# Kernel optimization log

Measured on AMD Instinct MI355X. Metric: run time of the kernel, lower is better.

The kernel has to match this reference:

```python
import jax, jax.numpy as jnp
import numpy as np

B, H, W, C = 4, 64, 64, 64
DK = C // 8  # key/query channels from Conv2D(filters=channels//8)


def setup_inputs() -> dict:
    key = jax.random.key(0)
    ks = jax.random.split(key, 4)
    x = jax.random.normal(ks[0], (B, H, W, C), dtype=jnp.float32)
    # he_normal-ish scale for 1x1 conv kernels (fan_in = C)
    s = np.sqrt(2.0 / C).astype(np.float32)
    Wf = jax.random.normal(ks[1], (C, DK), dtype=jnp.float32) * s
    Wg = jax.random.normal(ks[2], (C, DK), dtype=jnp.float32) * s
    Wh = jax.random.normal(ks[3], (C, C), dtype=jnp.float32) * s
    bf = jnp.zeros((DK,), dtype=jnp.float32)
    bg = jnp.zeros((DK,), dtype=jnp.float32)
    bh = jnp.zeros((C,), dtype=jnp.float32)
    return {"x": x, "Wf": Wf, "bf": bf, "Wg": Wg, "bg": bg, "Wh": Wh, "bh": bh}


def reference(x, Wf, bf, Wg, bg, Wh, bh):
    b, h, w, c = x.shape
    n = h * w
    xf = x.reshape(b, n, c)  # 1x1 conv == per-position linear over flattened spatial dims
    f = xf @ Wf + bf         # [B, N, DK]
    g = xf @ Wg + bg         # [B, N, DK]
    v = xf @ Wh + bh         # [B, N, C]
    # attention = softmax(g @ f^T) over keys (tf.nn.softmax default: last axis)
    scores = jnp.einsum('bnd,bmd->bnm', g, f)   # [B, N, N]
    attn = jax.nn.softmax(scores, axis=-1)
    out = jnp.einsum('bnm,bmc->bnc', attn, v)   # [B, N, C]
    return out
```

## Files before the change

### kernel.cpp

```cpp
#include <hip/hip_runtime.h>
#include <hip/hip_bf16.h>
#include <hip/hip_fp16.h>

typedef _Float16 half8_t  __attribute__((ext_vector_type(8)));
typedef short    short8_t __attribute__((ext_vector_type(8)));
typedef short    short4_t __attribute__((ext_vector_type(4)));
typedef float    f32x4    __attribute__((ext_vector_type(4)));

#define LOG2E 1.44269504088896f

__device__ __forceinline__ unsigned pack_bf16_2(float lo, float hi) {
  float2 f2; f2.x = lo; f2.y = hi;
  __hip_bfloat162 h2 = __float22bfloat162_rn(f2);
  return *reinterpret_cast<unsigned*>(&h2);
}

__global__ __launch_bounds__(512) void prep_kernel(
    const float* __restrict__ x,
    const float* __restrict__ Wf, const float* __restrict__ bf,
    const float* __restrict__ Wg, const float* __restrict__ bg,
    const float* __restrict__ Wh, const float* __restrict__ bh,
    _Float16* __restrict__ fh, _Float16* __restrict__ gh,
    unsigned short* __restrict__ vT)
{
  __shared__ _Float16 WtT[80 * 72];
  __shared__ float ball[80];
  const int t = threadIdx.x;

  {
    int c = t >> 3, d = t & 7;
    WtT[d * 72 + c]       = (_Float16)Wf[t];
    WtT[(8 + d) * 72 + c] = (_Float16)(Wg[t] * LOG2E);
  }
#pragma unroll
  for (int rep = 0; rep < 2; rep++) {
    int i4 = t + rep * 512;
    float4 wv4 = *(const float4*)(Wh + i4 * 4);
    int c  = i4 >> 4;
    int ch = (i4 & 15) * 4;
    WtT[(16 + ch + 0) * 72 + c] = (_Float16)wv4.x;
    WtT[(16 + ch + 1) * 72 + c] = (_Float16)wv4.y;
    WtT[(16 + ch + 2) * 72 + c] = (_Float16)wv4.z;
    WtT[(16 + ch + 3) * 72 + c] = (_Float16)wv4.w;
  }
  if (t < 80) ball[t] = (t < 8) ? bf[t] : (t < 16) ? bg[t - 8] * LOG2E : bh[t - 16];
  __syncthreads();

  const int lane = t & 63, wv = t >> 6;
  const int quad = lane >> 4, l15 = lane & 15;
  const int wr   = wv & 3;
  const int hsel = wv >> 2;
  const int p0  = blockIdx.x * 64;
  const int row = p0 + wr * 16 + l15;

  const float* xr = x + (size_t)row * 64 + quad * 8;
  float4 xa = *(const float4*)(xr);
  float4 xb = *(const float4*)(xr + 4);
  float4 xc = *(const float4*)(xr + 32);
  float4 xd = *(const float4*)(xr + 36);
  half8_t a0, a1;
  a0[0]=(_Float16)xa.x; a0[1]=(_Float16)xa.y; a0[2]=(_Float16)xa.z; a0[3]=(_Float16)xa.w;
  a0[4]=(_Float16)xb.x; a0[5]=(_Float16)xb.y; a0[6]=(_Float16)xb.z; a0[7]=(_Float16)xb.w;
  a1[0]=(_Float16)xc.x; a1[1]=(_Float16)xc.y; a1[2]=(_Float16)xc.z; a1[3]=(_Float16)xc.w;
  a1[4]=(_Float16)xd.x; a1[5]=(_Float16)xd.y; a1[6]=(_Float16)xd.z; a1[7]=(_Float16)xd.w;

  const f32x4 zc = {0.f, 0.f, 0.f, 0.f};
  const int b     = p0 >> 12;
  const int nbase = (p0 & 4095) + wr * 16 + quad * 4;
  const int kblock = nbase >> 5;
  const int r0     = nbase & 31;
  const int q8 = r0 >> 3, j8 = r0 & 7;
  const int slot0 = (j8 < 4) ? (q8 * 4 + j8) : (16 + q8 * 4 + (j8 - 4));
  const size_t fbase_out = ((size_t)b * 4096 + (kblock << 5) + slot0) * 8;
  const size_t gbase_out = ((size_t)p0 + wr * 16 + quad * 4) * 8;
  const size_t vbase_out = (((size_t)b * 128 + kblock) << 11) + r0;

  if (hsel == 0) {
    {
      const _Float16* wt = &WtT[l15 * 72 + quad * 8];
      half8_t b0 = *(const half8_t*)(wt);
      half8_t b1 = *(const half8_t*)(wt + 32);
      f32x4 d = __builtin_amdgcn_mfma_f32_16x16x32_f16(a0, b0, zc, 0, 0, 0);
      d = __builtin_amdgcn_mfma_f32_16x16x32_f16(a1, b1, d, 0, 0, 0);
      const float bias = ball[l15];
      if (l15 < 8) {
#pragma unroll
        for (int reg = 0; reg < 4; reg++)
          fh[fbase_out + (size_t)reg * 8 + l15] = (_Float16)(d[reg] + bias);
      } else {
#pragma unroll
        for (int reg = 0; reg < 4; reg++)
          gh[gbase_out + (size_t)reg * 8 + (l15 - 8)] = (_Float16)(d[reg] + bias);
      }
    }
#pragma unroll
    for (int nt = 1; nt < 3; nt++) {
      const int ch0 = nt * 16 + l15;
      const _Float16* wt = &WtT[ch0 * 72 + quad * 8];
      half8_t b0 = *(const half8_t*)(wt);
      half8_t b1 = *(const half8_t*)(wt + 32);
      f32x4 d = __builtin_amdgcn_mfma_f32_16x16x32_f16(a0, b0, zc, 0, 0, 0);
      d = __builtin_amdgcn_mfma_f32_16x16x32_f16(a1, b1, d, 0, 0, 0);
      const float bias = ball[ch0];
      const int vch = ch0 - 16;
      union { unsigned u[2]; short4_t s; } pk;
      pk.u[0] = pack_bf16_2(d[0] + bias, d[1] + bias);
      pk.u[1] = pack_bf16_2(d[2] + bias, d[3] + bias);
      *(short4_t*)(vT + vbase_out + (size_t)vch * 32) = pk.s;
    }
  } else {
#pragma unroll
    for (int nt = 3; nt < 5; nt++) {
      const int ch0 = nt * 16 + l15;
      const _Float16* wt = &WtT[ch0 * 72 + quad * 8];
      half8_t b0 = *(const half8_t*)(wt);
      half8_t b1 = *(const half8_t*)(wt + 32);
      f32x4 d = __builtin_amdgcn_mfma_f32_16x16x32_f16(a0, b0, zc, 0, 0, 0);
      d = __builtin_amdgcn_mfma_f32_16x16x32_f16(a1, b1, d, 0, 0, 0);
      const float bias = ball[ch0];
      const int vch = ch0 - 16;
      union { unsigned u[2]; short4_t s; } pk;
      pk.u[0] = pack_bf16_2(d[0] + bias, d[1] + bias);
      pk.u[1] = pack_bf16_2(d[2] + bias, d[3] + bias);
      *(short4_t*)(vT + vbase_out + (size_t)vch * 32) = pk.s;
    }
  }
}

__device__ __forceinline__ void compute_chunk(
    const half8_t& f0, const half8_t& f1,
    const short8_t& v0, const short8_t& v1,
    const short8_t& v2, const short8_t& v3,
    const half8_t (&gfrag)[4], const short8_t& ones8,
    f32x4 (&acc)[4][4], f32x4 (&acc4)[4])
{
  const f32x4 zc = {0.f, 0.f, 0.f, 0.f};
#pragma unroll
  for (int tt = 0; tt < 4; tt++) {
    f32x4 s0 = __builtin_amdgcn_mfma_f32_16x16x32_f16(f0, gfrag[tt], zc, 0, 0, 0);
    f32x4 s1 = __builtin_amdgcn_mfma_f32_16x16x32_f16(f1, gfrag[tt], zc, 0, 0, 0);
    float p00 = __builtin_amdgcn_exp2f(s0[0]), p01 = __builtin_amdgcn_exp2f(s0[1]);
    float p02 = __builtin_amdgcn_exp2f(s0[2]), p03 = __builtin_amdgcn_exp2f(s0[3]);
    float p10 = __builtin_amdgcn_exp2f(s1[0]), p11 = __builtin_amdgcn_exp2f(s1[1]);
    float p12 = __builtin_amdgcn_exp2f(s1[2]), p13 = __builtin_amdgcn_exp2f(s1[3]);
    union { unsigned u[4]; short8_t v; } pu;
    pu.u[0] = pack_bf16_2(p00, p01);
    pu.u[1] = pack_bf16_2(p02, p03);
    pu.u[2] = pack_bf16_2(p10, p11);
    pu.u[3] = pack_bf16_2(p12, p13);
    short8_t pfrag = pu.v;
    acc[tt][0] = __builtin_amdgcn_mfma_f32_16x16x32_bf16(v0, pfrag, acc[tt][0], 0, 0, 0);
    acc[tt][1] = __builtin_amdgcn_mfma_f32_16x16x32_bf16(v1, pfrag, acc[tt][1], 0, 0, 0);
    acc[tt][2] = __builtin_amdgcn_mfma_f32_16x16x32_bf16(v2, pfrag, acc[tt][2], 0, 0, 0);
    acc[tt][3] = __builtin_amdgcn_mfma_f32_16x16x32_bf16(v3, pfrag, acc[tt][3], 0, 0, 0);
    acc4[tt]   = __builtin_amdgcn_mfma_f32_16x16x32_bf16(ones8, pfrag, acc4[tt], 0, 0, 0);
  }
}

__global__ __launch_bounds__(512, 2) void attn_kernel(
    const _Float16* __restrict__ fh,
    const _Float16* __restrict__ gh,
    const unsigned short* __restrict__ vT,
    float* __restrict__ out)
{
  const int N    = 4096;
  const int lane = threadIdx.x & 63;
  const int w    = threadIdx.x >> 6;
  const int quad = lane >> 4;
  const int l15  = lane & 15;

  __shared__ float red[7][64][17];

  const int xcd = blockIdx.x & 7;
  const int b   = xcd >> 1;
  const int qg  = ((blockIdx.x >> 3) << 1) + (xcd & 1);
  const int q0  = qg * 64;
  const int kbase = w * 512;
  const int phase = (qg >> 1) & 15;

  const _Float16* fbase = fh + (size_t)b * N * 8;
  const _Float16* gbase = gh + (size_t)b * N * 8;
  const short*    vbat  = (const short*)vT + (size_t)b * 262144 + (l15 << 5) + (quad << 3);

  half8_t gfrag[4] = {{}, {}, {}, {}};
  if (quad == 0) {
#pragma unroll
    for (int tt = 0; tt < 4; tt++)
      gfrag[tt] = *(const half8_t*)(gbase + (size_t)(q0 + tt * 16 + l15) * 8);
  }

  const f32x4 zc = {0.f, 0.f, 0.f, 0.f};
  f32x4 acc[4][4];
  f32x4 acc4[4];
#pragma unroll
  for (int tt = 0; tt < 4; tt++) {
    acc4[tt] = zc;
#pragma unroll
    for (int ct = 0; ct < 4; ct++) acc[tt][ct] = zc;
  }

  short8_t ones8;
#pragma unroll
  for (int i = 0; i < 8; i++) ones8[i] = (short)0x3F80;

#define KOFF(j) (kbase + ((((j) + phase) & 15) << 5))
#define LOADC(k, F0, F1, V0, V1, V2, V3)                                  \
  {                                                                       \
    const int kk = (k);                                                   \
    if (quad == 0) {                                                      \
      F0 = *(const half8_t*)(fbase + (size_t)(kk + l15) * 8);             \
      F1 = *(const half8_t*)(fbase + (size_t)(kk + 16 + l15) * 8);        \
    }                                                                     \
    const short* vk = vbat + ((size_t)(kk >> 5) << 11);                   \
    V0 = *(const short8_t*)(vk);                                          \
    V1 = *(const short8_t*)(vk + 512);                                    \
    V2 = *(const short8_t*)(vk + 1024);                                   \
    V3 = *(const short8_t*)(vk + 1536);                                   \
  }

  half8_t  fA0 = {}, fA1 = {}, fB0 = {}, fB1 = {};
  half8_t  fC0 = {}, fC1 = {}, fD0 = {}, fD1 = {};
  short8_t vA0, vA1, vA2, vA3, vB0, vB1, vB2, vB3;
  short8_t vC0, vC1, vC2, vC3, vD0, vD1, vD2, vD3;

  LOADC(KOFF(0), fA0, fA1, vA0, vA1, vA2, vA3);
  LOADC(KOFF(1), fB0, fB1, vB0, vB1, vB2, vB3);

#pragma unroll 1
  for (int cc = 0; cc < 16; cc += 4) {
    LOADC(KOFF(cc + 2), fC0, fC1, vC0, vC1, vC2, vC3);
    LOADC(KOFF(cc + 3), fD0, fD1, vD0, vD1, vD2, vD3);
    compute_chunk(fA0, fA1, vA0, vA1, vA2, vA3, gfrag, ones8, acc, acc4);
    compute_chunk(fB0, fB1, vB0, vB1, vB2, vB3, gfrag, ones8, acc, acc4);
    if (cc + 4 < 16) {
      LOADC(KOFF(cc + 4), fA0, fA1, vA0, vA1, vA2, vA3);
      LOADC(KOFF(cc + 5), fB0, fB1, vB0, vB1, vB2, vB3);
    }
    compute_chunk(fC0, fC1, vC0, vC1, vC2, vC3, gfrag, ones8, acc, acc4);
    compute_chunk(fD0, fD1, vD0, vD1, vD2, vD3, gfrag, ones8, acc, acc4);
  }
#undef LOADC
#undef KOFF

#pragma unroll
  for (int tt = 0; tt < 4; tt++) {
    if (w > 0) {
      float* p = &red[w - 1][lane][0];
#pragma unroll
      for (int ct = 0; ct < 4; ct++)
#pragma unroll
        for (int reg = 0; reg < 4; reg++) p[ct * 4 + reg] = acc[tt][ct][reg];
      p[16] = acc4[tt][0];
    }
    __syncthreads();
    if (w == 0) {
#pragma unroll
      for (int ww = 0; ww < 7; ww++) {
        const float* p = &red[ww][lane][0];
#pragma unroll
        for (int reg = 0; reg < 4; reg++) {
          acc[tt][0][reg] += p[0 + reg];
          acc[tt][1][reg] += p[4 + reg];
          acc[tt][2][reg] += p[8 + reg];
          acc[tt][3][reg] += p[12 + reg];
        }
        acc4[tt][0] += p[16];
      }
    }
    if (tt < 3) __syncthreads();
  }

  if (w == 0) {
#pragma unroll
    for (int tt = 0; tt < 4; tt++) {
      const float inv = 1.0f / acc4[tt][0];
      float* ob = out + ((size_t)b * N + q0 + tt * 16 + l15) * 64 + (quad << 2);
      *(f32x4*)(ob)      = acc[tt][0] * inv;
      *(f32x4*)(ob + 16) = acc[tt][1] * inv;
      *(f32x4*)(ob + 32) = acc[tt][2] * inv;
      *(f32x4*)(ob + 48) = acc[tt][3] * inv;
    }
  }
}

extern "C" void kernel_launch(void* const* d_in, const int* in_sizes, int n_in,
                              void* d_out, int out_size, void* d_ws, size_t ws_size,
                              hipStream_t stream) {
  const float* x  = (const float*)d_in[0];
  const float* Wf = (const float*)d_in[1];
  const float* bf = (const float*)d_in[2];
  const float* Wg = (const float*)d_in[3];
  const float* bg = (const float*)d_in[4];
  const float* Wh = (const float*)d_in[5];
  const float* bh = (const float*)d_in[6];
  float* out = (float*)d_out;

  char* ws = (char*)d_ws;
  _Float16* fh = (_Float16*)ws;
  _Float16* gh = (_Float16*)(ws + 262144);
  unsigned short* vT = (unsigned short*)(ws + 524288);

  prep_kernel<<<256, 512, 0, stream>>>(x, Wf, bf, Wg, bg, Wh, bh, fh, gh, vT);
  attn_kernel<<<256, 512, 0, stream>>>(fh, gh, vT, out);
  attn_kernel<<<256, 512, 0, stream>>>(fh, gh, vT, out);
}
```

Baseline: 108.5 us.

## Fuse projection and attention into one kernel with a global atomic barrier

Merges the 1x1-conv projection kernel into the attention kernel, separated by a device-wide spin barrier on an atomic counter. The counter is reset with a memset each launch. This also drops the duplicated second attention launch. Shared memory is reused: a raw buffer first holds the transposed weights, then the reduction scratch. The barrier assumes all 256 blocks are co-resident, and a deadlock is possible if they are not.

```diff
diff --git a/kernel.cpp b/kernel.cpp
--- a/kernel.cpp
+++ b/kernel.cpp
@@ -13,118 +13,6 @@
   float2 f2; f2.x = lo; f2.y = hi;
   __hip_bfloat162 h2 = __float22bfloat162_rn(f2);
   return *reinterpret_cast<unsigned*>(&h2);
-}
-
-__global__ __launch_bounds__(512) void prep_kernel(
-    const float* __restrict__ x,
-    const float* __restrict__ Wf, const float* __restrict__ bf,
-    const float* __restrict__ Wg, const float* __restrict__ bg,
-    const float* __restrict__ Wh, const float* __restrict__ bh,
-    _Float16* __restrict__ fh, _Float16* __restrict__ gh,
-    unsigned short* __restrict__ vT)
-{
-  __shared__ _Float16 WtT[80 * 72];
-  __shared__ float ball[80];
-  const int t = threadIdx.x;
-
-  {
-    int c = t >> 3, d = t & 7;
-    WtT[d * 72 + c]       = (_Float16)Wf[t];
-    WtT[(8 + d) * 72 + c] = (_Float16)(Wg[t] * LOG2E);
-  }
-#pragma unroll
-  for (int rep = 0; rep < 2; rep++) {
-    int i4 = t + rep * 512;
-    float4 wv4 = *(const float4*)(Wh + i4 * 4);
-    int c  = i4 >> 4;
-    int ch = (i4 & 15) * 4;
-    WtT[(16 + ch + 0) * 72 + c] = (_Float16)wv4.x;
-    WtT[(16 + ch + 1) * 72 + c] = (_Float16)wv4.y;
-    WtT[(16 + ch + 2) * 72 + c] = (_Float16)wv4.z;
-    WtT[(16 + ch + 3) * 72 + c] = (_Float16)wv4.w;
-  }
-  if (t < 80) ball[t] = (t < 8) ? bf[t] : (t < 16) ? bg[t - 8] * LOG2E : bh[t - 16];
-  __syncthreads();
-
-  const int lane = t & 63, wv = t >> 6;
-  const int quad = lane >> 4, l15 = lane & 15;
-  const int wr   = wv & 3;
-  const int hsel = wv >> 2;
-  const int p0  = blockIdx.x * 64;
-  const int row = p0 + wr * 16 + l15;
-
-  const float* xr = x + (size_t)row * 64 + quad * 8;
-  float4 xa = *(const float4*)(xr);
-  float4 xb = *(const float4*)(xr + 4);
-  float4 xc = *(const float4*)(xr + 32);
-  float4 xd = *(const float4*)(xr + 36);
-  half8_t a0, a1;
-  a0[0]=(_Float16)xa.x; a0[1]=(_Float16)xa.y; a0[2]=(_Float16)xa.z; a0[3]=(_Float16)xa.w;
-  a0[4]=(_Float16)xb.x; a0[5]=(_Float16)xb.y; a0[6]=(_Float16)xb.z; a0[7]=(_Float16)xb.w;
-  a1[0]=(_Float16)xc.x; a1[1]=(_Float16)xc.y; a1[2]=(_Float16)xc.z; a1[3]=(_Float16)xc.w;
-  a1[4]=(_Float16)xd.x; a1[5]=(_Float16)xd.y; a1[6]=(_Float16)xd.z; a1[7]=(_Float16)xd.w;
-
-  const f32x4 zc = {0.f, 0.f, 0.f, 0.f};
-  const int b     = p0 >> 12;
-  const int nbase = (p0 & 4095) + wr * 16 + quad * 4;
-  const int kblock = nbase >> 5;
-  const int r0     = nbase & 31;
-  const int q8 = r0 >> 3, j8 = r0 & 7;
-  const int slot0 = (j8 < 4) ? (q8 * 4 + j8) : (16 + q8 * 4 + (j8 - 4));
-  const size_t fbase_out = ((size_t)b * 4096 + (kblock << 5) + slot0) * 8;
-  const size_t gbase_out = ((size_t)p0 + wr * 16 + quad * 4) * 8;
-  const size_t vbase_out = (((size_t)b * 128 + kblock) << 11) + r0;
-
-  if (hsel == 0) {
-    {
-      const _Float16* wt = &WtT[l15 * 72 + quad * 8];
-      half8_t b0 = *(const half8_t*)(wt);
-      half8_t b1 = *(const half8_t*)(wt + 32);
-      f32x4 d = __builtin_amdgcn_mfma_f32_16x16x32_f16(a0, b0, zc, 0, 0, 0);
-      d = __builtin_amdgcn_mfma_f32_16x16x32_f16(a1, b1, d, 0, 0, 0);
-      const float bias = ball[l15];
-      if (l15 < 8) {
-#pragma unroll
-        for (int reg = 0; reg < 4; reg++)
-          fh[fbase_out + (size_t)reg * 8 + l15] = (_Float16)(d[reg] + bias);
-      } else {
-#pragma unroll
-        for (int reg = 0; reg < 4; reg++)
-          gh[gbase_out + (size_t)reg * 8 + (l15 - 8)] = (_Float16)(d[reg] + bias);
-      }
-    }
-#pragma unroll
-    for (int nt = 1; nt < 3; nt++) {
-      const int ch0 = nt * 16 + l15;
-      const _Float16* wt = &WtT[ch0 * 72 + quad * 8];
-      half8_t b0 = *(const half8_t*)(wt);
-      half8_t b1 = *(const half8_t*)(wt + 32);
-      f32x4 d = __builtin_amdgcn_mfma_f32_16x16x32_f16(a0, b0, zc, 0, 0, 0);
-      d = __builtin_amdgcn_mfma_f32_16x16x32_f16(a1, b1, d, 0, 0, 0);
-      const float bias = ball[ch0];
-      const int vch = ch0 - 16;
-      union { unsigned u[2]; short4_t s; } pk;
-      pk.u[0] = pack_bf16_2(d[0] + bias, d[1] + bias);
-      pk.u[1] = pack_bf16_2(d[2] + bias, d[3] + bias);
-      *(short4_t*)(vT + vbase_out + (size_t)vch * 32) = pk.s;
-    }
-  } else {
-#pragma unroll
-    for (int nt = 3; nt < 5; nt++) {
-      const int ch0 = nt * 16 + l15;
-      const _Float16* wt = &WtT[ch0 * 72 + quad * 8];
-      half8_t b0 = *(const half8_t*)(wt);
-      half8_t b1 = *(const half8_t*)(wt + 32);
-      f32x4 d = __builtin_amdgcn_mfma_f32_16x16x32_f16(a0, b0, zc, 0, 0, 0);
-      d = __builtin_amdgcn_mfma_f32_16x16x32_f16(a1, b1, d, 0, 0, 0);
-      const float bias = ball[ch0];
-      const int vch = ch0 - 16;
-      union { unsigned u[2]; short4_t s; } pk;
-      pk.u[0] = pack_bf16_2(d[0] + bias, d[1] + bias);
-      pk.u[1] = pack_bf16_2(d[2] + bias, d[3] + bias);
-      *(short4_t*)(vT + vbase_out + (size_t)vch * 32) = pk.s;
-    }
-  }
 }
 
 __device__ __forceinline__ void compute_chunk(
@@ -157,19 +45,140 @@
   }
 }
 
-__global__ __launch_bounds__(512, 2) void attn_kernel(
-    const _Float16* __restrict__ fh,
-    const _Float16* __restrict__ gh,
-    const unsigned short* __restrict__ vT,
+__global__ __launch_bounds__(512, 2) void fused_kernel(
+    const float* __restrict__ x,
+    const float* __restrict__ Wf, const float* __restrict__ bf,
+    const float* __restrict__ Wg, const float* __restrict__ bg,
+    const float* __restrict__ Wh, const float* __restrict__ bh,
+    _Float16* __restrict__ fh, _Float16* __restrict__ gh,
+    unsigned short* __restrict__ vT,
+    unsigned* __restrict__ barrier_cnt,
     float* __restrict__ out)
 {
-  const int N    = 4096;
-  const int lane = threadIdx.x & 63;
-  const int w    = threadIdx.x >> 6;
+  __shared__ __align__(16) char smraw[7 * 64 * 17 * 4];
+
+  const int t    = threadIdx.x;
+  const int lane = t & 63;
+  const int wv   = t >> 6;
   const int quad = lane >> 4;
   const int l15  = lane & 15;
 
-  __shared__ float red[7][64][17];
+  {
+    _Float16* WtT  = (_Float16*)smraw;
+    float*    ball = (float*)(smraw + 80 * 72 * 2);
+
+    {
+      int c = t >> 3, d = t & 7;
+      WtT[d * 72 + c]       = (_Float16)Wf[t];
+      WtT[(8 + d) * 72 + c] = (_Float16)(Wg[t] * LOG2E);
+    }
+#pragma unroll
+    for (int rep = 0; rep < 2; rep++) {
+      int i4 = t + rep * 512;
+      float4 wv4 = *(const float4*)(Wh + i4 * 4);
+      int c  = i4 >> 4;
+      int ch = (i4 & 15) * 4;
+      WtT[(16 + ch + 0) * 72 + c] = (_Float16)wv4.x;
+      WtT[(16 + ch + 1) * 72 + c] = (_Float16)wv4.y;
+      WtT[(16 + ch + 2) * 72 + c] = (_Float16)wv4.z;
+      WtT[(16 + ch + 3) * 72 + c] = (_Float16)wv4.w;
+    }
+    if (t < 80) ball[t] = (t < 8) ? bf[t] : (t < 16) ? bg[t - 8] * LOG2E : bh[t - 16];
+    __syncthreads();
+
+    const int wr   = wv & 3;
+    const int hsel = wv >> 2;
+    const int p0  = blockIdx.x * 64;
+    const int row = p0 + wr * 16 + l15;
+
+    const float* xr = x + (size_t)row * 64 + quad * 8;
+    float4 xa = *(const float4*)(xr);
+    float4 xb = *(const float4*)(xr + 4);
+    float4 xc = *(const float4*)(xr + 32);
+    float4 xd = *(const float4*)(xr + 36);
+    half8_t a0, a1;
+    a0[0]=(_Float16)xa.x; a0[1]=(_Float16)xa.y; a0[2]=(_Float16)xa.z; a0[3]=(_Float16)xa.w;
+    a0[4]=(_Float16)xb.x; a0[5]=(_Float16)xb.y; a0[6]=(_Float16)xb.z; a0[7]=(_Float16)xb.w;
+    a1[0]=(_Float16)xc.x; a1[1]=(_Float16)xc.y; a1[2]=(_Float16)xc.z; a1[3]=(_Float16)xc.w;
+    a1[4]=(_Float16)xd.x; a1[5]=(_Float16)xd.y; a1[6]=(_Float16)xd.z; a1[7]=(_Float16)xd.w;
+
+    const f32x4 zc = {0.f, 0.f, 0.f, 0.f};
+    const int b     = p0 >> 12;
+    const int nbase = (p0 & 4095) + wr * 16 + quad * 4;
+    const int kblock = nbase >> 5;
+    const int r0     = nbase & 31;
+    const int q8 = r0 >> 3, j8 = r0 & 7;
+    const int slot0 = (j8 < 4) ? (q8 * 4 + j8) : (16 + q8 * 4 + (j8 - 4));
+    const size_t fbase_out = ((size_t)b * 4096 + (kblock << 5) + slot0) * 8;
+    const size_t gbase_out = ((size_t)p0 + wr * 16 + quad * 4) * 8;
+    const size_t vbase_out = (((size_t)b * 128 + kblock) << 11) + r0;
+
+    if (hsel == 0) {
+      {
+        const _Float16* wt = &WtT[l15 * 72 + quad * 8];
+        half8_t b0 = *(const half8_t*)(wt);
+        half8_t b1 = *(const half8_t*)(wt + 32);
+        f32x4 d = __builtin_amdgcn_mfma_f32_16x16x32_f16(a0, b0, zc, 0, 0, 0);
+        d = __builtin_amdgcn_mfma_f32_16x16x32_f16(a1, b1, d, 0, 0, 0);
+        const float bias = ball[l15];
+        if (l15 < 8) {
+#pragma unroll
+          for (int reg = 0; reg < 4; reg++)
+            fh[fbase_out + (size_t)reg * 8 + l15] = (_Float16)(d[reg] + bias);
+        } else {
+#pragma unroll
+          for (int reg = 0; reg < 4; reg++)
+            gh[gbase_out + (size_t)reg * 8 + (l15 - 8)] = (_Float16)(d[reg] + bias);
+        }
+      }
+#pragma unroll
+      for (int nt = 1; nt < 3; nt++) {
+        const int ch0 = nt * 16 + l15;
+        const _Float16* wt = &WtT[ch0 * 72 + quad * 8];
+        half8_t b0 = *(const half8_t*)(wt);
+        half8_t b1 = *(const half8_t*)(wt + 32);
+        f32x4 d = __builtin_amdgcn_mfma_f32_16x16x32_f16(a0, b0, zc, 0, 0, 0);
+        d = __builtin_amdgcn_mfma_f32_16x16x32_f16(a1, b1, d, 0, 0, 0);
+        const float bias = ball[ch0];
+        const int vch = ch0 - 16;
+        union { unsigned u[2]; short4_t s; } pk;
+        pk.u[0] = pack_bf16_2(d[0] + bias, d[1] + bias);
+        pk.u[1] = pack_bf16_2(d[2] + bias, d[3] + bias);
+        *(short4_t*)(vT + vbase_out + (size_t)vch * 32) = pk.s;
+      }
+    } else {
+#pragma unroll
+      for (int nt = 3; nt < 5; nt++) {
+        const int ch0 = nt * 16 + l15;
+        const _Float16* wt = &WtT[ch0 * 72 + quad * 8];
+        half8_t b0 = *(const half8_t*)(wt);
+        half8_t b1 = *(const half8_t*)(wt + 32);
+        f32x4 d = __builtin_amdgcn_mfma_f32_16x16x32_f16(a0, b0, zc, 0, 0, 0);
+        d = __builtin_amdgcn_mfma_f32_16x16x32_f16(a1, b1, d, 0, 0, 0);
+        const float bias = ball[ch0];
+        const int vch = ch0 - 16;
+        union { unsigned u[2]; short4_t s; } pk;
+        pk.u[0] = pack_bf16_2(d[0] + bias, d[1] + bias);
+        pk.u[1] = pack_bf16_2(d[2] + bias, d[3] + bias);
+        *(short4_t*)(vT + vbase_out + (size_t)vch * 32) = pk.s;
+      }
+    }
+  }
+
+  __threadfence();
+  __syncthreads();
+  if (t == 0) {
+    __hip_atomic_fetch_add(barrier_cnt, 1u, __ATOMIC_ACQ_REL, __HIP_MEMORY_SCOPE_AGENT);
+    while (__hip_atomic_load(barrier_cnt, __ATOMIC_ACQUIRE, __HIP_MEMORY_SCOPE_AGENT) < 256u) {
+      __builtin_amdgcn_s_sleep(2);
+    }
+  }
+  __syncthreads();
+  __threadfence();
+
+  const int N    = 4096;
+  const int w    = wv;
+  float* red = (float*)smraw;
 
   const int xcd = blockIdx.x & 7;
   const int b   = xcd >> 1;
@@ -242,10 +251,11 @@
 #undef LOADC
 #undef KOFF
 
+  __syncthreads();
 #pragma unroll
   for (int tt = 0; tt < 4; tt++) {
     if (w > 0) {
-      float* p = &red[w - 1][lane][0];
+      float* p = &red[((w - 1) * 64 + lane) * 17];
 #pragma unroll
       for (int ct = 0; ct < 4; ct++)
 #pragma unroll
@@ -256,7 +266,7 @@
     if (w == 0) {
 #pragma unroll
       for (int ww = 0; ww < 7; ww++) {
-        const float* p = &red[ww][lane][0];
+        const float* p = &red[(ww * 64 + lane) * 17];
 #pragma unroll
         for (int reg = 0; reg < 4; reg++) {
           acc[tt][0][reg] += p[0 + reg];
@@ -299,8 +309,10 @@
   _Float16* fh = (_Float16*)ws;
   _Float16* gh = (_Float16*)(ws + 262144);
   unsigned short* vT = (unsigned short*)(ws + 524288);
-
-  prep_kernel<<<256, 512, 0, stream>>>(x, Wf, bf, Wg, bg, Wh, bh, fh, gh, vT);
-  attn_kernel<<<256, 512, 0, stream>>>(fh, gh, vT, out);
-  attn_kernel<<<256, 512, 0, stream>>>(fh, gh, vT, out);
+  unsigned* barrier_cnt = (unsigned*)(ws + 3145728);
+
+  hipMemsetAsync(barrier_cnt, 0, 64, stream);
+
+  fused_kernel<<<256, 512, 0, stream>>>(x, Wf, bf, Wg, bg, Wh, bh,
+                                        fh, gh, vT, barrier_cnt, out);
 }
```

New measurement: 191.1 us. +76.1%, slower.
